# Optimization experiments

Measured on AMD Instinct MI355X. Metric: run time of the kernel, lower is better.

The kernel has to match this reference:

```python
import jax, jax.numpy as jnp
import numpy as np
from jax import lax

SHIFT_SIZE = 5
PAD = SHIFT_SIZE // 2


def _chunk_shifts(C):
    # torch.chunk(x, 5, dim=1): chunk size = ceil(C/5); shift for chunk i is i - PAD
    csz = -(-C // SHIFT_SIZE)
    return jnp.arange(C) // csz - PAD  # (C,) in [-PAD, PAD]


def _shift_along_h(x, shifts):
    # x: (B,C,H,W). Equivalent of pad+chunk+roll(dim=2)+cat+narrow: per-channel
    # zero-filled shift along H (no wraparound since |shift| <= PAD).
    B, C, H, W = x.shape
    xp = jnp.pad(x, ((0, 0), (0, 0), (PAD, PAD), (0, 0)))
    c_idx = jnp.arange(C)[:, None]              # (C,1)
    h_idx = jnp.arange(H)[None, :] + PAD - shifts[:, None]  # (C,H)
    return xp[:, c_idx, h_idx, :]               # (B,C,H,W)


def _shift_along_w(x, shifts):
    return jnp.swapaxes(_shift_along_h(jnp.swapaxes(x, 2, 3), shifts), 2, 3)


def setup_inputs() -> dict:
    key = jax.random.key(0)
    ks = jax.random.split(key, 7)
    B, H, W, C, hidden = 8, 128, 128, 256, 256
    x = jax.random.normal(ks[0], (B, H * W, C), dtype=jnp.float32)
    w1 = jax.random.normal(ks[1], (hidden, C), dtype=jnp.float32) * 0.02
    b1 = jnp.zeros((hidden,), dtype=jnp.float32)
    fan_out = 3 * 3 * hidden // hidden  # groups = hidden
    dw_w = jax.random.normal(ks[2], (hidden, 1, 3, 3), dtype=jnp.float32) * np.sqrt(2.0 / fan_out)
    dw_b = jnp.zeros((hidden,), dtype=jnp.float32)
    w2 = jax.random.normal(ks[3], (C, hidden), dtype=jnp.float32) * 0.02
    b2 = jnp.zeros((C,), dtype=jnp.float32)
    return {"x": x, "H": H, "W": W, "w1": w1, "b1": b1,
            "dw_w": dw_w, "dw_b": dw_b, "w2": w2, "b2": b2}


def reference(x, H, W, w1, b1, dw_w, dw_b, w2, b2):
    B, N, C = x.shape
    shifts = _chunk_shifts(C)

    # --- shift along H, then fc1 ---
    xn = jnp.reshape(jnp.swapaxes(x, 1, 2), (B, C, H, W))
    x_s = _shift_along_h(xn, shifts)
    x_s = jnp.swapaxes(x_s.reshape(B, C, H * W), 1, 2)   # (B,N,C)
    h = x_s @ w1.T + b1                                  # (B,N,hidden)

    # --- depthwise 3x3 conv ---
    Ch = h.shape[-1]
    himg = jnp.reshape(jnp.swapaxes(h, 1, 2), (B, Ch, H, W))
    himg = lax.conv_general_dilated(
        himg, dw_w, window_strides=(1, 1), padding=((1, 1), (1, 1)),
        feature_group_count=Ch,
        dimension_numbers=("NCHW", "OIHW", "NCHW")) + dw_b[None, :, None, None]
    h = jnp.swapaxes(himg.reshape(B, Ch, H * W), 1, 2)

    h = jax.nn.gelu(h, approximate=False)

    # --- shift along W, then fc2 ---
    hn = jnp.reshape(jnp.swapaxes(h, 1, 2), (B, Ch, H, W))
    h_s = _shift_along_w(hn, _chunk_shifts(Ch))
    h_s = jnp.swapaxes(h_s.reshape(B, Ch, H * W), 1, 2)  # (B,N,hidden)
    out = h_s @ w2.T + b2                                # (B,N,C)
    return out
```

## Files before the change

### kernel.cpp

```cpp
#include <hip/hip_runtime.h>
#include <hip/hip_bf16.h>
#include <math.h>

#define Hc   128
#define Wc   128
#define Cc   256
#define Nc   (Hc * Wc)
#define Bn   8
#define Mtot (Bn * Nc)
#define CSZ  52
#define SPAD 2

typedef unsigned short ushort4v __attribute__((ext_vector_type(4)));
typedef unsigned short ushort8  __attribute__((ext_vector_type(8)));
typedef __bf16         bf16x8   __attribute__((ext_vector_type(8)));
typedef float          f32x4    __attribute__((ext_vector_type(4)));

__device__ __forceinline__ float bf2f(unsigned short u) {
    return __uint_as_float(((unsigned)u) << 16);
}
__device__ __forceinline__ unsigned short f2bf(float f) {
    unsigned u = __float_as_uint(f);
    return (unsigned short)((u + 0x7fffu + ((u >> 16) & 1u)) >> 16);
}
__device__ __forceinline__ unsigned pk2bf(float a, float b) {
    unsigned ua = __float_as_uint(a) + 0x8000u;
    unsigned ub = __float_as_uint(b) + 0x8000u;
    return __builtin_amdgcn_perm(ub, ua, 0x07060302);
}
__device__ __forceinline__ void async16(const void* g, void* l) {
    __builtin_amdgcn_global_load_lds(
        (const __attribute__((address_space(1))) unsigned*)g,
        (__attribute__((address_space(3))) unsigned*)l, 16, 0, 0);
}

__global__ __launch_bounds__(256)
void wprep_kernel(const float* __restrict__ w1, const float* __restrict__ dw_w,
                  unsigned short* __restrict__ w1b, float* __restrict__ dwT)
{
    const int g = blockIdx.x * 256 + threadIdx.x;
    {
        float4 a = *(const float4*)(w1 + (size_t)g * 4);
        ushort4v o = { f2bf(a.x), f2bf(a.y), f2bf(a.z), f2bf(a.w) };
        *(ushort4v*)(w1b + (size_t)g * 4) = o;
    }
    if (g < 9 * Cc) dwT[(g % 9) * Cc + g / 9] = dw_w[g];
}

__global__ __launch_bounds__(256)
void fc1_mfma_kernel(const float* __restrict__ x, const unsigned short* __restrict__ w1b,
                     const float* __restrict__ b1, unsigned short* __restrict__ h1)
{
    __shared__ __align__(16) unsigned char smem[36864];
    __bf16* As = (__bf16*)smem;
    __bf16* Bs = (__bf16*)(smem + 20480);
    unsigned short* Cs = (unsigned short*)smem;

    const int tid  = threadIdx.x;
    const int lane = tid & 63;
    const int wave = tid >> 6;
    const int wm = (wave >> 1) * 64, wn = (wave & 1) * 64;

    const int lid = ((blockIdx.x & 7) << 8) | (blockIdx.x >> 3);
    const int bx  = lid >> 1;
    const int j0  = (lid & 1) * 128;
    const size_t m0 = (size_t)bx * 128;
    const int bb = bx >> 7, hh = bx & 127;
    const int r = tid >> 1, half = tid & 1;
    const int idx0 = tid, idx1 = tid + 256;

    float4 av[4];
    auto loadA = [&](int t) {
        const int kb = t * 32 + half * 16;
#pragma unroll
        for (int j = 0; j < 4; ++j) {
            const int c  = kb + j * 4;
            const int s  = c / CSZ - SPAD;
            const int hs = hh - s;
            av[j] = make_float4(0.f, 0.f, 0.f, 0.f);
            if (hs >= 0 && hs < Hc)
                av[j] = *(const float4*)(x + ((size_t)(bb * Nc + hs * Wc + r)) * Cc + c);
        }
    };
    auto storeA = [&](int buf) {
        uint4 q0, q1;
        q0.x = pk2bf(av[0].x, av[0].y); q0.y = pk2bf(av[0].z, av[0].w);
        q0.z = pk2bf(av[1].x, av[1].y); q0.w = pk2bf(av[1].z, av[1].w);
        q1.x = pk2bf(av[2].x, av[2].y); q1.y = pk2bf(av[2].z, av[2].w);
        q1.z = pk2bf(av[3].x, av[3].y); q1.w = pk2bf(av[3].z, av[3].w);
        __bf16* dst = As + buf * (128 * 40) + r * 40 + half * 16;
        *(uint4*)dst       = q0;
        *(uint4*)(dst + 8) = q1;
    };
    auto stageB = [&](int buf, int t) {
        const int k0 = t * 32;
        __bf16* bdst = Bs + buf * (128 * 32);
        async16(w1b + (size_t)(j0 + (idx0 >> 2)) * Cc + k0 + (idx0 & 3) * 8, bdst + idx0 * 8);
        async16(w1b + (size_t)(j0 + (idx1 >> 2)) * Cc + k0 + (idx1 & 3) * 8, bdst + idx1 * 8);
    };

    f32x4 acc[4][4] = {};

    loadA(0);
    stageB(0, 0);
    storeA(0);
    __syncthreads();

    const int kq = (lane >> 4) * 8;
    const int rr = lane & 15;
    int cur = 0;
    for (int t = 0; t < 8; ++t) {
        const int nxt = cur ^ 1;
        if (t < 7) {
            loadA(t + 1);
            stageB(nxt, t + 1);
        }
        bf16x8 a[4], b[4];
        const __bf16* ap = As + cur * (128 * 40);
        const __bf16* bp = Bs + cur * (128 * 32);
#pragma unroll
        for (int i = 0; i < 4; ++i) {
            a[i] = *(const bf16x8*)(ap + (wm + i * 16 + rr) * 40 + kq);
            b[i] = *(const bf16x8*)(bp + (wn + i * 16 + rr) * 32 + kq);
        }
#pragma unroll
        for (int i = 0; i < 4; ++i)
#pragma unroll
            for (int j = 0; j < 4; ++j)
                acc[i][j] = __builtin_amdgcn_mfma_f32_16x16x32_bf16(a[i], b[j], acc[i][j], 0, 0, 0);
        if (t < 7) storeA(nxt);
        __syncthreads();
        cur = nxt;
    }

    const int cq = (lane >> 4) * 4;
    const int cc = lane & 15;
    float bv[4];
#pragma unroll
    for (int j = 0; j < 4; ++j) bv[j] = b1[j0 + wn + j * 16 + cc];
#pragma unroll
    for (int i = 0; i < 4; ++i)
#pragma unroll
        for (int j = 0; j < 4; ++j) {
            const int col = wn + j * 16 + cc;
#pragma unroll
            for (int rg = 0; rg < 4; ++rg)
                Cs[(wm + i * 16 + cq + rg) * 136 + col] = f2bf(acc[i][j][rg] + bv[j]);
        }
    __syncthreads();
    {
        const int row = tid >> 1, hf = tid & 1;
        const unsigned short* src = Cs + row * 136 + hf * 64;
        unsigned short* dst = h1 + (m0 + row) * Cc + j0 + hf * 64;
#pragma unroll
        for (int i = 0; i < 8; ++i)
            *(uint4*)(dst + i * 8) = *(const uint4*)(src + i * 8);
    }
}

__global__ __launch_bounds__(256)
void zero_borders_kernel(unsigned short* __restrict__ gsh)
{
    const int gid = blockIdx.x * 256 + threadIdx.x;
    const int cg  = gid & 31;
    const int rest = gid >> 5;
    const int wi = rest & 3;
    const int bh = rest >> 2;
    const int w  = (wi & 2) ? (wi + 124) : wi;
    uint4 z; z.x = z.y = z.z = z.w = 0u;
    *(uint4*)(gsh + ((size_t)bh * 128 + w) * Cc + cg * 8) = z;
}

__global__ __launch_bounds__(256)
void dwconv_gelu_scatter_kernel(const unsigned short* __restrict__ h1,
                                const float* __restrict__ dwT, const float* __restrict__ dw_b,
                                unsigned short* __restrict__ gsh)
{
    const int t   = threadIdx.x;
    const int cg  = t & 31;
    const int wq  = t >> 5;
    const int c0  = cg * 8;
    const int bh  = blockIdx.x >> 2;
    const int qtr = blockIdx.x & 3;
    const int bb  = bh >> 7, hh = bh & 127;
    const size_t rowb = (size_t)bb * Nc + (size_t)hh * Wc;
    const int wbase = qtr * 32 + wq * 4 - 1;

    float acc[4][8];
    {
        float4 a0 = *(const float4*)(dw_b + c0);
        float4 a1 = *(const float4*)(dw_b + c0 + 4);
#pragma unroll
        for (int i = 0; i < 4; ++i) {
            acc[i][0] = a0.x; acc[i][1] = a0.y; acc[i][2] = a0.z; acc[i][3] = a0.w;
            acc[i][4] = a1.x; acc[i][5] = a1.y; acc[i][6] = a1.z; acc[i][7] = a1.w;
        }
    }

#pragma unroll
    for (int dy = -1; dy <= 1; ++dy) {
        const int y = hh + dy;
        if (y < 0 || y >= Hc) continue;
        const unsigned short* rp = h1 + ((size_t)bb * Nc + (size_t)y * Wc) * Cc + c0;
        float in[6][8];
#pragma unroll
        for (int dx = 0; dx < 6; ++dx) {
            const int w = wbase + dx;
            ushort8 raw = {0, 0, 0, 0, 0, 0, 0, 0};
            if (w >= 0 && w < Wc) raw = *(const ushort8*)(rp + (size_t)w * Cc);
#pragma unroll
            for (int c = 0; c < 8; ++c) in[dx][c] = bf2f(raw[c]);
        }
        const float* wrow = dwT + (dy + 1) * 3 * Cc + c0;
        float wr[3][8];
#pragma unroll
        for (int tx = 0; tx < 3; ++tx) {
            float4 wa = *(const float4*)(wrow + tx * Cc);
            float4 wb = *(const float4*)(wrow + tx * Cc + 4);
            wr[tx][0] = wa.x; wr[tx][1] = wa.y; wr[tx][2] = wa.z; wr[tx][3] = wa.w;
            wr[tx][4] = wb.x; wr[tx][5] = wb.y; wr[tx][6] = wb.z; wr[tx][7] = wb.w;
        }
#pragma unroll
        for (int i = 0; i < 4; ++i)
#pragma unroll
            for (int tx = 0; tx < 3; ++tx)
#pragma unroll
                for (int c = 0; c < 8; ++c)
                    acc[i][c] += in[i + tx][c] * wr[tx][c];
    }

    const int s0 = c0 / CSZ - SPAD;
    const int s1 = (c0 + 4) / CSZ - SPAD;
#pragma unroll
    for (int i = 0; i < 4; ++i) {
        float g[8];
#pragma unroll
        for (int c = 0; c < 8; ++c) {
            const float v = acc[i][c];
            const float u = v * v;
            const float a = __builtin_fmaf(0.0713548162f, u, 1.5957691216f);
            const float e = __expf(v * a);
            g[c] = v * e * __builtin_amdgcn_rcpf(e + 1.0f);
        }
        uint2 lo, hi;
        lo.x = pk2bf(g[0], g[1]); lo.y = pk2bf(g[2], g[3]);
        hi.x = pk2bf(g[4], g[5]); hi.y = pk2bf(g[6], g[7]);
        const int wo = wbase + 1 + i;
        const int w0 = wo + s0, w1 = wo + s1;
        if ((unsigned)w0 < (unsigned)Wc) *(uint2*)(gsh + (rowb + w0) * Cc + c0)     = lo;
        if ((unsigned)w1 < (unsigned)Wc) *(uint2*)(gsh + (rowb + w1) * Cc + c0 + 4) = hi;
    }
}

__global__ __launch_bounds__(256)
void fc2_mfma_kernel(const unsigned short* __restrict__ A, const float* __restrict__ w2,
                     const float* __restrict__ b2, float* __restrict__ out)
{
    __shared__ __align__(16) unsigned char smem[36864];
    __bf16* As = (__bf16*)smem;
    __bf16* Bs = (__bf16*)(smem + 16384);

    const int tid  = threadIdx.x;
    const int lane = tid & 63;
    const int wave = tid >> 6;
    const int wm = (wave >> 1) * 64, wn = (wave & 1) * 64;

    const int lid = ((blockIdx.x & 7) << 8) | (blockIdx.x >> 3);
    const size_t m0 = (size_t)(lid >> 1) * 128;
    const int j0 = (lid & 1) * 128;

    const int idx0 = tid, idx1 = tid + 256;
    const int brow = tid >> 1, bch = (tid & 1) * 16;

    float4 wv[4];
    auto loadB = [&](int t) {
        const float* src = w2 + (size_t)(j0 + brow) * Cc + t * 32 + bch;
        wv[0] = *(const float4*)(src);
        wv[1] = *(const float4*)(src + 4);
        wv[2] = *(const float4*)(src + 8);
        wv[3] = *(const float4*)(src + 12);
    };
    auto storeB = [&](int buf) {
        uint4 p0, p1;
        p0.x = pk2bf(wv[0].x, wv[0].y); p0.y = pk2bf(wv[0].z, wv[0].w);
        p0.z = pk2bf(wv[1].x, wv[1].y); p0.w = pk2bf(wv[1].z, wv[1].w);
        p1.x = pk2bf(wv[2].x, wv[2].y); p1.y = pk2bf(wv[2].z, wv[2].w);
        p1.z = pk2bf(wv[3].x, wv[3].y); p1.w = pk2bf(wv[3].z, wv[3].w);
        __bf16* dst = Bs + buf * (128 * 40) + brow * 40 + bch;
        *(uint4*)dst       = p0;
        *(uint4*)(dst + 8) = p1;
    };
    auto stageA = [&](int buf, int t) {
        const int k0 = t * 32;
        __bf16* adst = As + buf * (128 * 32);
        async16(A + (m0 + (idx0 >> 2)) * Cc + k0 + (idx0 & 3) * 8, adst + idx0 * 8);
        async16(A + (m0 + (idx1 >> 2)) * Cc + k0 + (idx1 & 3) * 8, adst + idx1 * 8);
    };

    f32x4 acc[4][4] = {};

    loadB(0);
    stageA(0, 0);
    storeB(0);
    __syncthreads();

    const int kq = (lane >> 4) * 8;
    const int rr = lane & 15;
    int cur = 0;
    for (int t = 0; t < 8; ++t) {
        const int nxt = cur ^ 1;
        if (t < 7) {
            loadB(t + 1);
            stageA(nxt, t + 1);
        }
        bf16x8 a[4], b[4];
        const __bf16* ap = As + cur * (128 * 32);
        const __bf16* bp = Bs + cur * (128 * 40);
#pragma unroll
        for (int i = 0; i < 4; ++i) {
            a[i] = *(const bf16x8*)(ap + (wm + i * 16 + rr) * 32 + kq);
            b[i] = *(const bf16x8*)(bp + (wn + i * 16 + rr) * 40 + kq);
        }
#pragma unroll
        for (int i = 0; i < 4; ++i)
#pragma unroll
            for (int j = 0; j < 4; ++j)
                acc[i][j] = __builtin_amdgcn_mfma_f32_16x16x32_bf16(a[i], b[j], acc[i][j], 0, 0, 0);
        if (t < 7) storeB(nxt);
        __syncthreads();
        cur = nxt;
    }

    const int cq = (lane >> 4) * 4;
    const int cc = lane & 15;
    float bv[4];
#pragma unroll
    for (int j = 0; j < 4; ++j) bv[j] = b2[j0 + wn + j * 16 + cc];
#pragma unroll
    for (int i = 0; i < 4; ++i)
#pragma unroll
        for (int j = 0; j < 4; ++j) {
            const int col = j0 + wn + j * 16 + cc;
#pragma unroll
            for (int rg = 0; rg < 4; ++rg)
                out[(m0 + wm + i * 16 + cq + rg) * Cc + col] = acc[i][j][rg] + bv[j];
        }
}

extern "C" void kernel_launch(void* const* d_in, const int* in_sizes, int n_in,
                              void* d_out, int out_size, void* d_ws, size_t ws_size,
                              hipStream_t stream) {
    const float* x    = (const float*)d_in[0];
    const float* w1   = (const float*)d_in[3];
    const float* b1   = (const float*)d_in[4];
    const float* dw_w = (const float*)d_in[5];
    const float* dw_b = (const float*)d_in[6];
    const float* w2   = (const float*)d_in[7];
    const float* b2   = (const float*)d_in[8];
    float* out = (float*)d_out;

    unsigned short* h1  = (unsigned short*)d_ws;
    unsigned short* gsh = h1 + (size_t)Mtot * Cc;
    unsigned short* w1b = (unsigned short*)d_out;
    float*          dwT = (float*)(w1b + 65536);

    wprep_kernel<<<dim3(64), dim3(256), 0, stream>>>(w1, dw_w, w1b, dwT);
    fc1_mfma_kernel<<<dim3(2 * Mtot / 128), dim3(256), 0, stream>>>(x, w1b, b1, h1);
    zero_borders_kernel<<<dim3(512), dim3(256), 0, stream>>>(gsh);
    dwconv_gelu_scatter_kernel<<<dim3(4 * Mtot / 128), dim3(256), 0, stream>>>(h1, dwT, dw_b, gsh);
    fc2_mfma_kernel<<<dim3(2 * Mtot / 128), dim3(256), 0, stream>>>(gsh, w2, b2, out);
}
```

Baseline: 357.9 us.

## Deepen fc1/fc2 GEMM pipelines with triple-buffered async loads and XOR-swizzled LDS

Both MFMA GEMM kernels now keep the async global-to-LDS operand in a three-stage ring, prefetched two k-steps ahead. Each step ends with a hand-written s_waitcnt vmcnt(N)+s_barrier instead of __syncthreads, so only the oldest loads are waited on. The padded LDS rows (stride 40) are replaced by unpadded stride-32 rows with an XOR swizzle to avoid bank conflicts, and the k-loop is fully unrolled by macro. The aim is to hide global load latency and cut LDS conflicts, at the cost of more LDS per block, which may reduce occupancy, and fragile manual vmcnt counting.

```diff
diff --git a/kernel.cpp b/kernel.cpp
--- a/kernel.cpp
+++ b/kernel.cpp
@@ -33,6 +33,8 @@
         (const __attribute__((address_space(1))) unsigned*)g,
         (__attribute__((address_space(3))) unsigned*)l, 16, 0, 0);
 }
+
+#define FENCE(vm) asm volatile("s_waitcnt vmcnt(" #vm ") lgkmcnt(0)\n\ts_barrier" ::: "memory")
 
 __global__ __launch_bounds__(256)
 void wprep_kernel(const float* __restrict__ w1, const float* __restrict__ dw_w,
@@ -51,9 +53,9 @@
 void fc1_mfma_kernel(const float* __restrict__ x, const unsigned short* __restrict__ w1b,
                      const float* __restrict__ b1, unsigned short* __restrict__ h1)
 {
-    __shared__ __align__(16) unsigned char smem[36864];
+    __shared__ __align__(16) unsigned char smem[40960];
     __bf16* As = (__bf16*)smem;
-    __bf16* Bs = (__bf16*)(smem + 20480);
+    __bf16* Bs = (__bf16*)(smem + 16384);
     unsigned short* Cs = (unsigned short*)smem;
 
     const int tid  = threadIdx.x;
@@ -69,8 +71,17 @@
     const int r = tid >> 1, half = tid & 1;
     const int idx0 = tid, idx1 = tid + 256;
 
-    float4 av[4];
-    auto loadA = [&](int t) {
+    const int xr  = (r >> 2) & 3;
+    const int sA0 = ((half * 2 + 0) ^ xr) * 8;
+    const int sA1 = ((half * 2 + 1) ^ xr) * 8;
+    const int bxo0 = ((idx0 & 3) ^ ((idx0 >> 4) & 3)) * 8;
+    const int bxo1 = ((idx1 & 3) ^ ((idx1 >> 4) & 3)) * 8;
+    const size_t bro0 = (size_t)(j0 + (idx0 >> 2)) * Cc;
+    const size_t bro1 = (size_t)(j0 + (idx1 >> 2)) * Cc;
+
+    float4 av0[4], av1[4];
+
+    auto loadA = [&](int t, float4* av) {
         const int kb = t * 32 + half * 16;
 #pragma unroll
         for (int j = 0; j < 4; ++j) {
@@ -82,56 +93,64 @@
                 av[j] = *(const float4*)(x + ((size_t)(bb * Nc + hs * Wc + r)) * Cc + c);
         }
     };
-    auto storeA = [&](int buf) {
+    auto storeA = [&](int buf, const float4* av) {
         uint4 q0, q1;
         q0.x = pk2bf(av[0].x, av[0].y); q0.y = pk2bf(av[0].z, av[0].w);
         q0.z = pk2bf(av[1].x, av[1].y); q0.w = pk2bf(av[1].z, av[1].w);
         q1.x = pk2bf(av[2].x, av[2].y); q1.y = pk2bf(av[2].z, av[2].w);
         q1.z = pk2bf(av[3].x, av[3].y); q1.w = pk2bf(av[3].z, av[3].w);
-        __bf16* dst = As + buf * (128 * 40) + r * 40 + half * 16;
-        *(uint4*)dst       = q0;
-        *(uint4*)(dst + 8) = q1;
+        __bf16* base = As + buf * 4096 + r * 32;
+        *(uint4*)(base + sA0) = q0;
+        *(uint4*)(base + sA1) = q1;
     };
     auto stageB = [&](int buf, int t) {
         const int k0 = t * 32;
-        __bf16* bdst = Bs + buf * (128 * 32);
-        async16(w1b + (size_t)(j0 + (idx0 >> 2)) * Cc + k0 + (idx0 & 3) * 8, bdst + idx0 * 8);
-        async16(w1b + (size_t)(j0 + (idx1 >> 2)) * Cc + k0 + (idx1 & 3) * 8, bdst + idx1 * 8);
+        __bf16* bdst = Bs + buf * 4096;
+        async16(w1b + bro0 + k0 + bxo0, bdst + idx0 * 8);
+        async16(w1b + bro1 + k0 + bxo1, bdst + idx1 * 8);
     };
 
     f32x4 acc[4][4] = {};
-
-    loadA(0);
+    const int kq  = (lane >> 4) * 8;
+    const int kqx = kq ^ (((lane >> 2) & 3) << 3);
+    const int rr  = lane & 15;
+
+    loadA(0, av0);
     stageB(0, 0);
-    storeA(0);
-    __syncthreads();
-
-    const int kq = (lane >> 4) * 8;
-    const int rr = lane & 15;
-    int cur = 0;
-    for (int t = 0; t < 8; ++t) {
-        const int nxt = cur ^ 1;
-        if (t < 7) {
-            loadA(t + 1);
-            stageB(nxt, t + 1);
-        }
-        bf16x8 a[4], b[4];
-        const __bf16* ap = As + cur * (128 * 40);
-        const __bf16* bp = Bs + cur * (128 * 32);
-#pragma unroll
-        for (int i = 0; i < 4; ++i) {
-            a[i] = *(const bf16x8*)(ap + (wm + i * 16 + rr) * 40 + kq);
-            b[i] = *(const bf16x8*)(bp + (wn + i * 16 + rr) * 32 + kq);
-        }
-#pragma unroll
-        for (int i = 0; i < 4; ++i)
-#pragma unroll
-            for (int j = 0; j < 4; ++j)
-                acc[i][j] = __builtin_amdgcn_mfma_f32_16x16x32_bf16(a[i], b[j], acc[i][j], 0, 0, 0);
-        if (t < 7) storeA(nxt);
-        __syncthreads();
-        cur = nxt;
-    }
+    stageB(1, 1);
+    loadA(1, av1);
+    storeA(0, av0);
+    FENCE(6);
+
+#define F1_STEP(T, AVL, AVS, FN)                                              \
+    {                                                                          \
+        if constexpr ((T) <= 5) { loadA((T) + 2, AVL); stageB(((T) + 2) % 3, (T) + 2); } \
+        bf16x8 a[4], b[4];                                                     \
+        const __bf16* ap = As + ((T) & 1) * 4096;                              \
+        const __bf16* bp = Bs + ((T) % 3) * 4096;                              \
+        _Pragma("unroll")                                                      \
+        for (int i = 0; i < 4; ++i) {                                          \
+            a[i] = *(const bf16x8*)(ap + (wm + i * 16 + rr) * 32 + kqx);       \
+            b[i] = *(const bf16x8*)(bp + (wn + i * 16 + rr) * 32 + kqx);       \
+        }                                                                      \
+        _Pragma("unroll")                                                      \
+        for (int i = 0; i < 4; ++i)                                            \
+            _Pragma("unroll")                                                  \
+            for (int j = 0; j < 4; ++j)                                        \
+                acc[i][j] = __builtin_amdgcn_mfma_f32_16x16x32_bf16(a[i], b[j], acc[i][j], 0, 0, 0); \
+        if constexpr ((T) <= 6) storeA(((T) + 1) & 1, AVS);                    \
+        FN;                                                                    \
+    }
+
+    F1_STEP(0, av0, av1, FENCE(6));
+    F1_STEP(1, av1, av0, FENCE(6));
+    F1_STEP(2, av0, av1, FENCE(6));
+    F1_STEP(3, av1, av0, FENCE(6));
+    F1_STEP(4, av0, av1, FENCE(6));
+    F1_STEP(5, av1, av0, FENCE(6));
+    F1_STEP(6, av0, av1, FENCE(0));
+    F1_STEP(7, av1, av0, FENCE(0));
+#undef F1_STEP
 
     const int cq = (lane >> 4) * 4;
     const int cc = lane & 15;
@@ -256,9 +275,9 @@
 void fc2_mfma_kernel(const unsigned short* __restrict__ A, const float* __restrict__ w2,
                      const float* __restrict__ b2, float* __restrict__ out)
 {
-    __shared__ __align__(16) unsigned char smem[36864];
+    __shared__ __align__(16) unsigned char smem[40960];
     __bf16* As = (__bf16*)smem;
-    __bf16* Bs = (__bf16*)(smem + 16384);
+    __bf16* Bs = (__bf16*)(smem + 24576);
 
     const int tid  = threadIdx.x;
     const int lane = tid & 63;
@@ -270,11 +289,19 @@
     const int j0 = (lid & 1) * 128;
 
     const int idx0 = tid, idx1 = tid + 256;
-    const int brow = tid >> 1, bch = (tid & 1) * 16;
+    const int brow = tid >> 1, bhalf = tid & 1;
+
+    const int axo0 = ((idx0 & 3) ^ ((idx0 >> 4) & 3)) * 8;
+    const int axo1 = ((idx1 & 3) ^ ((idx1 >> 4) & 3)) * 8;
+    const size_t aro0 = (m0 + (idx0 >> 2)) * Cc;
+    const size_t aro1 = (m0 + (idx1 >> 2)) * Cc;
+    const int xrB = (brow >> 2) & 3;
+    const int sB0 = ((bhalf * 2 + 0) ^ xrB) * 8;
+    const int sB1 = ((bhalf * 2 + 1) ^ xrB) * 8;
 
     float4 wv[4];
     auto loadB = [&](int t) {
-        const float* src = w2 + (size_t)(j0 + brow) * Cc + t * 32 + bch;
+        const float* src = w2 + (size_t)(j0 + brow) * Cc + t * 32 + bhalf * 16;
         wv[0] = *(const float4*)(src);
         wv[1] = *(const float4*)(src + 4);
         wv[2] = *(const float4*)(src + 8);
@@ -286,50 +313,58 @@
         p0.z = pk2bf(wv[1].x, wv[1].y); p0.w = pk2bf(wv[1].z, wv[1].w);
         p1.x = pk2bf(wv[2].x, wv[2].y); p1.y = pk2bf(wv[2].z, wv[2].w);
         p1.z = pk2bf(wv[3].x, wv[3].y); p1.w = pk2bf(wv[3].z, wv[3].w);
-        __bf16* dst = Bs + buf * (128 * 40) + brow * 40 + bch;
-        *(uint4*)dst       = p0;
-        *(uint4*)(dst + 8) = p1;
+        __bf16* base = Bs + buf * 4096 + brow * 32;
+        *(uint4*)(base + sB0) = p0;
+        *(uint4*)(base + sB1) = p1;
     };
     auto stageA = [&](int buf, int t) {
         const int k0 = t * 32;
-        __bf16* adst = As + buf * (128 * 32);
-        async16(A + (m0 + (idx0 >> 2)) * Cc + k0 + (idx0 & 3) * 8, adst + idx0 * 8);
-        async16(A + (m0 + (idx1 >> 2)) * Cc + k0 + (idx1 & 3) * 8, adst + idx1 * 8);
+        __bf16* adst = As + buf * 4096;
+        async16(A + aro0 + k0 + axo0, adst + idx0 * 8);
+        async16(A + aro1 + k0 + axo1, adst + idx1 * 8);
     };
 
     f32x4 acc[4][4] = {};
+    const int kq  = (lane >> 4) * 8;
+    const int kqx = kq ^ (((lane >> 2) & 3) << 3);
+    const int rr  = lane & 15;
 
     loadB(0);
     stageA(0, 0);
+    stageA(1, 1);
     storeB(0);
-    __syncthreads();
-
-    const int kq = (lane >> 4) * 8;
-    const int rr = lane & 15;
-    int cur = 0;
-    for (int t = 0; t < 8; ++t) {
-        const int nxt = cur ^ 1;
-        if (t < 7) {
-            loadB(t + 1);
-            stageA(nxt, t + 1);
-        }
-        bf16x8 a[4], b[4];
-        const __bf16* ap = As + cur * (128 * 32);
-        const __bf16* bp = Bs + cur * (128 * 40);
-#pragma unroll
-        for (int i = 0; i < 4; ++i) {
-            a[i] = *(const bf16x8*)(ap + (wm + i * 16 + rr) * 32 + kq);
-            b[i] = *(const bf16x8*)(bp + (wn + i * 16 + rr) * 40 + kq);
-        }
-#pragma unroll
-        for (int i = 0; i < 4; ++i)
-#pragma unroll
-            for (int j = 0; j < 4; ++j)
-                acc[i][j] = __builtin_amdgcn_mfma_f32_16x16x32_bf16(a[i], b[j], acc[i][j], 0, 0, 0);
-        if (t < 7) storeB(nxt);
-        __syncthreads();
-        cur = nxt;
-    }
+    FENCE(2);
+
+#define F2_STEP(T, FN)                                                        \
+    {                                                                          \
+        if constexpr ((T) <= 6) loadB((T) + 1);                                \
+        if constexpr ((T) <= 5) stageA(((T) + 2) % 3, (T) + 2);                \
+        bf16x8 a[4], b[4];                                                     \
+        const __bf16* ap = As + ((T) % 3) * 4096;                              \
+        const __bf16* bp = Bs + ((T) & 1) * 4096;                              \
+        _Pragma("unroll")                                                      \
+        for (int i = 0; i < 4; ++i) {                                          \
+            a[i] = *(const bf16x8*)(ap + (wm + i * 16 + rr) * 32 + kqx);       \
+            b[i] = *(const bf16x8*)(bp + (wn + i * 16 + rr) * 32 + kqx);       \
+        }                                                                      \
+        _Pragma("unroll")                                                      \
+        for (int i = 0; i < 4; ++i)                                            \
+            _Pragma("unroll")                                                  \
+            for (int j = 0; j < 4; ++j)                                        \
+                acc[i][j] = __builtin_amdgcn_mfma_f32_16x16x32_bf16(a[i], b[j], acc[i][j], 0, 0, 0); \
+        if constexpr ((T) <= 6) storeB(((T) + 1) & 1);                         \
+        FN;                                                                    \
+    }
+
+    F2_STEP(0, FENCE(2));
+    F2_STEP(1, FENCE(2));
+    F2_STEP(2, FENCE(2));
+    F2_STEP(3, FENCE(2));
+    F2_STEP(4, FENCE(2));
+    F2_STEP(5, FENCE(2));
+    F2_STEP(6, FENCE(0));
+    F2_STEP(7, FENCE(0));
+#undef F2_STEP
 
     const int cq = (lane >> 4) * 4;
     const int cc = lane & 15;
```

New measurement: 359.5 us. Within noise of the previous version (+0.4%).
